# Kernel tuning notes

Hardware: AMD Instinct MI355X
Metric: run time of the kernel (lower is better)

The kernel has to match this reference:

```python
import jax, jax.numpy as jnp
import numpy as np

N, DIN, DH, DOUT, E, K = 8192, 1024, 4096, 1024, 8, 2
AUX_EPS = 1e-10


def setup_inputs() -> dict:
    key = jax.random.key(0)
    kx, kgw, kgb, kw1, kb1, kw2, kb2 = jax.random.split(key, 7)
    def init(k, shape, fan_in):
        return (jax.random.normal(k, shape, jnp.float32) / np.sqrt(fan_in)).astype(jnp.float32)
    return {
        "x": jax.random.normal(kx, (N, DIN), jnp.float32),
        "gate_w": init(kgw, (DIN, E), DIN),
        "gate_b": jnp.zeros((E,), jnp.float32),
        "w1": init(kw1, (E, DIN, DH), DIN),
        "b1": jnp.zeros((E, DH), jnp.float32),
        "w2": init(kw2, (E, DH, DOUT), DH),
        "b2": jnp.zeros((E, DOUT), jnp.float32),
    }


def reference(x, gate_w, gate_b, w1, b1, w2, b2):
    # Gating
    logits = x @ gate_w + gate_b                      # [N, E]
    probs = jax.nn.softmax(logits, axis=-1)           # [N, E]
    topk_vals, topk_idx = jax.lax.top_k(probs, K)     # [N, K]
    topk_norm = topk_vals / (topk_vals.sum(-1, keepdims=True) + AUX_EPS)

    # Scatter normalized top-k weights into a dense [N, E] combine matrix.
    n = x.shape[0]
    weights = jnp.zeros((n, E), x.dtype).at[jnp.arange(n)[:, None], topk_idx].add(topk_norm)

    # Dense all-expert FFN (same math: non-selected experts get weight 0).
    h = jax.nn.relu(jnp.einsum('nd,edh->neh', x, w1) + b1)   # [N, E, DH]
    y = jnp.einsum('neh,eho->neo', h, w2) + b2               # [N, E, DOUT]
    output = jnp.einsum('neo,ne->no', y, weights)            # [N, DOUT]

    # Aux load-balancing loss: KL(mean_probs || uniform)
    mean_probs = probs.mean(axis=0)
    aux_loss = jnp.sum(mean_probs * jnp.log(mean_probs * E + AUX_EPS))

    return output, aux_loss, probs
```

## Files before the change

kernel.cpp:

```cpp
#include <hip/hip_runtime.h>

#define NTOK 8192
#define DIN 1024
#define DH   4096
#define DOUT 1024
#define NE   8
#define MAXTILES 136
#define SLOTCAP  (MAXTILES*128)

typedef __bf16 bf16x8 __attribute__((ext_vector_type(8)));
typedef float  f32x4  __attribute__((ext_vector_type(4)));

constexpr size_t OFF_W1T  = 0;
constexpr size_t OFF_W2T  = 67108864;
constexpr size_t OFF_XB   = 134217728;
constexpr size_t OFF_H    = 150994944;
constexpr size_t OFF_SROW = 293601280;
constexpr size_t OFF_SW   = 293670912;
constexpr size_t OFF_TIDX = 293740544;
constexpr size_t OFF_TW   = 293806080;
constexpr size_t OFF_CTRL = 293871616;
constexpr size_t OFF_PART = 293871744;

__device__ __forceinline__ ushort f2bf(float f){
  unsigned u = __float_as_uint(f);
  u += 0x7fff + ((u >> 16) & 1);
  return (ushort)(u >> 16);
}

#define GLDS(g,l) __builtin_amdgcn_global_load_lds( \
    (const __attribute__((address_space(1))) void*)(g), \
    (__attribute__((address_space(3))) void*)(l), 16, 0, 0)

__global__ void k_cvt_x(const float4* __restrict__ x, ushort4* __restrict__ xb){
  int i = blockIdx.x * 256 + threadIdx.x;
  float4 v = x[i];
  ushort4 o;
  o.x = f2bf(v.x); o.y = f2bf(v.y); o.z = f2bf(v.z); o.w = f2bf(v.w);
  xb[i] = o;
}

__global__ void k_transpose(const float* __restrict__ W, ushort* __restrict__ WT, int R, int C){
  __shared__ ushort tl[64][65];
  int e  = blockIdx.z;
  int r0 = blockIdx.x * 64, c0 = blockIdx.y * 64;
  const float* Wp  = W  + (size_t)e * R * C;
  ushort*      WTp = WT + (size_t)e * R * C;
  int tr = threadIdx.x >> 6, tc = threadIdx.x & 63;
#pragma unroll
  for (int i = 0; i < 16; i++){
    int r = tr + i * 4;
    tl[r][tc] = f2bf(Wp[(size_t)(r0 + r) * C + c0 + tc]);
  }
  __syncthreads();
#pragma unroll
  for (int i = 0; i < 16; i++){
    int r = tr + i * 4;
    WTp[(size_t)(c0 + r) * R + r0 + tc] = tl[tc][r];
  }
}

__global__ void k_gate(const float* __restrict__ x, const float* __restrict__ gw,
                       const float* __restrict__ gb, float* __restrict__ probs_out,
                       int* __restrict__ topk_idx, float* __restrict__ topk_w,
                       int* __restrict__ count, float* __restrict__ partial){
  __shared__ float psum[8];
  __shared__ int   pcnt[8];
  int wv = threadIdx.x >> 6, lane = threadIdx.x & 63;
  int row = blockIdx.x * 4 + wv;
  if (threadIdx.x < 8){ psum[threadIdx.x] = 0.f; pcnt[threadIdx.x] = 0; }
  __syncthreads();

  const float4* x4 = (const float4*)(x + (size_t)row * DIN);
  float acc[8];
#pragma unroll
  for (int e = 0; e < 8; e++) acc[e] = 0.f;
#pragma unroll
  for (int j = 0; j < 4; j++){
    float4 v = x4[j * 64 + lane];
    int kbase = (j * 64 + lane) * 4;
#pragma unroll
    for (int c = 0; c < 4; c++){
      float xv = (&v.x)[c];
      const float4* g4 = (const float4*)(gw + (size_t)(kbase + c) * 8);
      float4 g0 = g4[0], g1 = g4[1];
      acc[0] += xv * g0.x; acc[1] += xv * g0.y; acc[2] += xv * g0.z; acc[3] += xv * g0.w;
      acc[4] += xv * g1.x; acc[5] += xv * g1.y; acc[6] += xv * g1.z; acc[7] += xv * g1.w;
    }
  }
#pragma unroll
  for (int e = 0; e < 8; e++)
#pragma unroll
    for (int off = 32; off; off >>= 1) acc[e] += __shfl_xor(acc[e], off, 64);

  float lg[8], p[8], mx = -1e30f, s = 0.f;
#pragma unroll
  for (int e = 0; e < 8; e++){ lg[e] = acc[e] + gb[e]; mx = fmaxf(mx, lg[e]); }
#pragma unroll
  for (int e = 0; e < 8; e++){ p[e] = expf(lg[e] - mx); s += p[e]; }
  float inv = 1.f / s;
#pragma unroll
  for (int e = 0; e < 8; e++) p[e] *= inv;

  if (lane < 8) probs_out[(size_t)row * 8 + lane] = p[lane];

  if (lane == 0){
    int i1 = 0; float v1 = p[0];
#pragma unroll
    for (int e = 1; e < 8; e++) if (p[e] > v1){ v1 = p[e]; i1 = e; }
    int i2 = -1; float v2 = -1.f;
#pragma unroll
    for (int e = 0; e < 8; e++){ if (e == i1) continue; if (p[e] > v2){ v2 = p[e]; i2 = e; } }
    float denom = 1.f / (v1 + v2 + 1e-10f);
    topk_idx[row * 2]     = i1;  topk_idx[row * 2 + 1] = i2;
    topk_w  [row * 2]     = v1 * denom;  topk_w[row * 2 + 1] = v2 * denom;
    atomicAdd(&pcnt[i1], 1); atomicAdd(&pcnt[i2], 1);
  }
  if (lane < 8) atomicAdd(&psum[lane], p[lane]);
  __syncthreads();
  if (threadIdx.x < 8){
    partial[(size_t)blockIdx.x * 8 + threadIdx.x] = psum[threadIdx.x];
    if (pcnt[threadIdx.x]) atomicAdd(&count[threadIdx.x], pcnt[threadIdx.x]);
  }
}

__global__ void k_aux(const float* __restrict__ partial, const int* __restrict__ count,
                      float* __restrict__ aux_out, int* __restrict__ tile_off){
  __shared__ float red[256];
  __shared__ float tot[8];
  int t = threadIdx.x, e = t & 7;
  float s = 0.f;
  for (int b = (t >> 3); b < 2048; b += 32) s += partial[(size_t)b * 8 + e];
  red[t] = s; __syncthreads();
  if (t < 8){ float v = 0.f; for (int c = 0; c < 32; c++) v += red[c * 8 + t]; tot[t] = v; }
  __syncthreads();
  if (t == 0){
    float aux = 0.f;
    for (int i = 0; i < 8; i++){
      float m = tot[i] * (1.f / 8192.f);
      aux += m * logf(m * 8.f + 1e-10f);
    }
    aux_out[0] = aux;
    int off = 0;
    for (int i = 0; i < 8; i++){ tile_off[i] = off; off += (count[i] + 127) >> 7; }
    tile_off[8] = off;
  }
}

__global__ void k_scatter(const int* __restrict__ topk_idx, const float* __restrict__ topk_w,
                          const int* __restrict__ tile_off, int* __restrict__ fill,
                          int* __restrict__ slot_row, float* __restrict__ slot_w){
  int i = blockIdx.x * 256 + threadIdx.x;
  int row = i >> 1;
  int e = topk_idx[i];
  float w = topk_w[i];
  int lane = threadIdx.x & 63;
  int pos = 0;
#pragma unroll
  for (int ex = 0; ex < 8; ex++){
    unsigned long long mask = __ballot(e == ex);
    if (e == ex){
      int leader = __ffsll((long long)mask) - 1;
      int base = 0;
      if (lane == leader) base = atomicAdd(&fill[ex], (int)__popcll(mask));
      base = __shfl(base, leader, 64);
      pos = base + (int)__popcll(mask & ((1ull << lane) - 1ull));
    }
  }
  int slot = tile_off[e] * 128 + pos;
  slot_row[slot] = row;
  slot_w[slot]   = w;
}

__global__ __launch_bounds__(256) void k_gemm1(
    const ushort* __restrict__ xb, const ushort* __restrict__ w1t,
    const float* __restrict__ b1, const int* __restrict__ slot_row,
    const int* __restrict__ tile_off, ushort* __restrict__ H){
  __shared__ ushort As[128 * 32];
  __shared__ ushort Bs[128 * 32];
  int tileM = blockIdx.x, tileN = blockIdx.y;
  if (tileM >= tile_off[8]) return;
  int e = 0;
  while (e < 7 && tile_off[e + 1] <= tileM) e++;
  int m0 = tileM * 128, n0 = tileN * 128;
  int t = threadIdx.x;

  const ushort* aBase[2]; const ushort* bBase[2];
#pragma unroll
  for (int i = 0; i < 2; i++){
    int c = i * 256 + t, r = c >> 2, cc = c & 3;
    aBase[i] = xb  + (size_t)slot_row[m0 + r] * DIN + cc * 8;
    bBase[i] = w1t + ((size_t)e * DH + n0 + r) * DIN + cc * 8;
  }
  int wv = t >> 6, lane = t & 63;
  int wm = wv >> 1, wn = wv & 1, quad = lane >> 4, lc = lane & 15;
  f32x4 acc[4][4] = {};

  for (int k0 = 0; k0 < DIN; k0 += 32){
#pragma unroll
    for (int i = 0; i < 2; i++){
      int c = i * 256 + t;
      GLDS(aBase[i] + k0, As + c * 8);
      GLDS(bBase[i] + k0, Bs + c * 8);
    }
    __syncthreads();
    bf16x8 a[4], b[4];
#pragma unroll
    for (int i = 0; i < 4; i++) a[i] = *(const bf16x8*)(As + (wm * 64 + i * 16 + lc) * 32 + quad * 8);
#pragma unroll
    for (int j = 0; j < 4; j++) b[j] = *(const bf16x8*)(Bs + (wn * 64 + j * 16 + lc) * 32 + quad * 8);
#pragma unroll
    for (int i = 0; i < 4; i++)
#pragma unroll
      for (int j = 0; j < 4; j++)
        acc[i][j] = __builtin_amdgcn_mfma_f32_16x16x32_bf16(a[i], b[j], acc[i][j], 0, 0, 0);
    __syncthreads();
  }

  const float* b1e = b1 + (size_t)e * DH;
#pragma unroll
  for (int i = 0; i < 4; i++){
#pragma unroll
    for (int r = 0; r < 4; r++){
      int slot = m0 + wm * 64 + i * 16 + quad * 4 + r;
      ushort* hrow = H + (size_t)slot * DH;
#pragma unroll
      for (int j = 0; j < 4; j++){
        int col = n0 + wn * 64 + j * 16 + lc;
        float v = acc[i][j][r] + b1e[col];
        hrow[col] = f2bf(fmaxf(v, 0.f));
      }
    }
  }
}

__global__ __launch_bounds__(256) void k_gemm2(
    const ushort* __restrict__ H, const ushort* __restrict__ w2t,
    const float* __restrict__ b2, const int* __restrict__ slot_row,
    const float* __restrict__ slot_w, const int* __restrict__ tile_off,
    float* __restrict__ out){
  __shared__ ushort As[128 * 32];
  __shared__ ushort Bs[128 * 32];
  int tileM = blockIdx.x, tileN = blockIdx.y;
  if (tileM >= tile_off[8]) return;
  int e = 0;
  while (e < 7 && tile_off[e + 1] <= tileM) e++;
  int m0 = tileM * 128, n0 = tileN * 128;
  int t = threadIdx.x;

  const ushort* aBase[2]; const ushort* bBase[2];
#pragma unroll
  for (int i = 0; i < 2; i++){
    int c = i * 256 + t, r = c >> 2, cc = c & 3;
    aBase[i] = H   + (size_t)(m0 + r) * DH + cc * 8;
    bBase[i] = w2t + ((size_t)e * DOUT + n0 + r) * DH + cc * 8;
  }
  int wv = t >> 6, lane = t & 63;
  int wm = wv >> 1, wn = wv & 1, quad = lane >> 4, lc = lane & 15;
  f32x4 acc[4][4] = {};

  for (int k0 = 0; k0 < DH; k0 += 32){
#pragma unroll
    for (int i = 0; i < 2; i++){
      int c = i * 256 + t;
      GLDS(aBase[i] + k0, As + c * 8);
      GLDS(bBase[i] + k0, Bs + c * 8);
    }
    __syncthreads();
    bf16x8 a[4], b[4];
#pragma unroll
    for (int i = 0; i < 4; i++) a[i] = *(const bf16x8*)(As + (wm * 64 + i * 16 + lc) * 32 + quad * 8);
#pragma unroll
    for (int j = 0; j < 4; j++) b[j] = *(const bf16x8*)(Bs + (wn * 64 + j * 16 + lc) * 32 + quad * 8);
#pragma unroll
    for (int i = 0; i < 4; i++)
#pragma unroll
      for (int j = 0; j < 4; j++)
        acc[i][j] = __builtin_amdgcn_mfma_f32_16x16x32_bf16(a[i], b[j], acc[i][j], 0, 0, 0);
    __syncthreads();
  }

  const float* b2e = b2 + (size_t)e * DOUT;
#pragma unroll
  for (int i = 0; i < 4; i++){
#pragma unroll
    for (int r = 0; r < 4; r++){
      int slot = m0 + wm * 64 + i * 16 + quad * 4 + r;
      float w = slot_w[slot];
      if (w == 0.f) continue;
      float* orow = out + (size_t)slot_row[slot] * DOUT;
#pragma unroll
      for (int j = 0; j < 4; j++){
        int col = n0 + wn * 64 + j * 16 + lc;
        atomicAdd(orow + col, w * (acc[i][j][r] + b2e[col]));
      }
    }
  }
}

extern "C" void kernel_launch(void* const* d_in, const int* in_sizes, int n_in,
                              void* d_out, int out_size, void* d_ws, size_t ws_size,
                              hipStream_t stream){
  const float* x      = (const float*)d_in[0];
  const float* gate_w = (const float*)d_in[1];
  const float* gate_b = (const float*)d_in[2];
  const float* w1     = (const float*)d_in[3];
  const float* b1     = (const float*)d_in[4];
  const float* w2     = (const float*)d_in[5];
  const float* b2     = (const float*)d_in[6];
  float* out = (float*)d_out;

  char* ws = (char*)d_ws;
  ushort* W1T   = (ushort*)(ws + OFF_W1T);
  ushort* W2T   = (ushort*)(ws + OFF_W2T);
  ushort* XB    = (ushort*)(ws + OFF_XB);
  ushort* H     = (ushort*)(ws + OFF_H);
  int*    SROW  = (int*)   (ws + OFF_SROW);
  float*  SW    = (float*) (ws + OFF_SW);
  int*    TIDX  = (int*)   (ws + OFF_TIDX);
  float*  TW    = (float*) (ws + OFF_TW);
  int*    COUNT = (int*)   (ws + OFF_CTRL);
  int*    FILL  = (int*)   (ws + OFF_CTRL + 32);
  int*    TOFF  = (int*)   (ws + OFF_CTRL + 64);
  float*  PART  = (float*) (ws + OFF_PART);

  float* aux_out   = out + (size_t)NTOK * DOUT;
  float* probs_out = aux_out + 1;

  hipMemsetAsync(d_out, 0, (size_t)out_size * 4, stream);
  hipMemsetAsync(ws + OFF_CTRL, 0, 128, stream);
  hipMemsetAsync(ws + OFF_SROW, 0, (size_t)SLOTCAP * 8, stream);

  k_cvt_x<<<dim3((NTOK * DIN / 4) / 256), 256, 0, stream>>>((const float4*)x, (ushort4*)XB);
  k_transpose<<<dim3(DIN / 64, DH / 64, NE), 256, 0, stream>>>(w1, W1T, DIN, DH);
  k_transpose<<<dim3(DH / 64, DOUT / 64, NE), 256, 0, stream>>>(w2, W2T, DH, DOUT);
  k_gate<<<dim3(NTOK / 4), 256, 0, stream>>>(x, gate_w, gate_b, probs_out, TIDX, TW, COUNT, PART);
  k_aux<<<dim3(1), 256, 0, stream>>>(PART, COUNT, aux_out, TOFF);
  k_scatter<<<dim3(NTOK * 2 / 256), 256, 0, stream>>>(TIDX, TW, TOFF, FILL, SROW, SW);
  k_gemm1<<<dim3(MAXTILES, DH / 128), 256, 0, stream>>>(XB, W1T, b1, SROW, TOFF, H);
  k_gemm2<<<dim3(MAXTILES, DOUT / 128), 256, 0, stream>>>(H, W2T, b2, SROW, SW, TOFF, out);
}
```

Measured before the change: 990.4 us.

## Replace grouped GEMMs with 256-row tiled, double-buffered, swizzled 8-wave kernel

Both expert GEMMs now use one templated kernel with 256-row M tiles, 512 threads, a double-buffered LDS pipeline with XOR-swizzled layout, staged global-to-LDS prefetch interleaved with MFMA clusters, s_setprio, and an XCD-aware block remap. Routing tiles are padded to 256 rows, and the W1/W2 transposed buffers now share one workspace region, with the W2 transpose run after GEMM1. The aim is more data reuse per tile, fewer LDS bank conflicts and hidden load latency. The cost is extra padding waste per expert and higher register pressure.

Result: slower. 1.353 ms (+36.6%).

```diff
diff --git a/kernel.cpp b/kernel.cpp
--- a/kernel.cpp
+++ b/kernel.cpp
@@ -1,26 +1,25 @@
 #include <hip/hip_runtime.h>
 
 #define NTOK 8192
-#define DIN 1024
+#define DIN  1024
 #define DH   4096
 #define DOUT 1024
 #define NE   8
-#define MAXTILES 136
-#define SLOTCAP  (MAXTILES*128)
+#define MAXT 72
+#define SLOTCAP (MAXT*256)
 
 typedef __bf16 bf16x8 __attribute__((ext_vector_type(8)));
 typedef float  f32x4  __attribute__((ext_vector_type(4)));
 
-constexpr size_t OFF_W1T  = 0;
-constexpr size_t OFF_W2T  = 67108864;
-constexpr size_t OFF_XB   = 134217728;
-constexpr size_t OFF_H    = 150994944;
-constexpr size_t OFF_SROW = 293601280;
-constexpr size_t OFF_SW   = 293670912;
-constexpr size_t OFF_TIDX = 293740544;
-constexpr size_t OFF_TW   = 293806080;
-constexpr size_t OFF_CTRL = 293871616;
-constexpr size_t OFF_PART = 293871744;
+constexpr size_t OFF_WT   = 0;
+constexpr size_t OFF_XB   = 67108864;
+constexpr size_t OFF_H    = 83886080;
+constexpr size_t OFF_SROW = 234881024;
+constexpr size_t OFF_SW   = 234954752;
+constexpr size_t OFF_TIDX = 235028480;
+constexpr size_t OFF_TW   = 235094016;
+constexpr size_t OFF_CTRL = 235159552;
+constexpr size_t OFF_PART = 235159680;
 
 __device__ __forceinline__ ushort f2bf(float f){
   unsigned u = __float_as_uint(f);
@@ -31,6 +30,10 @@
 #define GLDS(g,l) __builtin_amdgcn_global_load_lds( \
     (const __attribute__((address_space(1))) void*)(g), \
     (__attribute__((address_space(3))) void*)(l), 16, 0, 0)
+
+#define SBAR __builtin_amdgcn_sched_barrier(0)
+#define WBAR __builtin_amdgcn_s_barrier()
+#define VMCNT(n) asm volatile("s_waitcnt vmcnt(" #n ")" ::: "memory")
 
 __global__ void k_cvt_x(const float4* __restrict__ x, ushort4* __restrict__ xb){
   int i = blockIdx.x * 256 + threadIdx.x;
@@ -142,7 +145,7 @@
     }
     aux_out[0] = aux;
     int off = 0;
-    for (int i = 0; i < 8; i++){ tile_off[i] = off; off += (count[i] + 127) >> 7; }
+    for (int i = 0; i < 8; i++){ tile_off[i] = off; off += (count[i] + 255) >> 8; }
     tile_off[8] = off;
   }
 }
@@ -167,134 +170,172 @@
       pos = base + (int)__popcll(mask & ((1ull << lane) - 1ull));
     }
   }
-  int slot = tile_off[e] * 128 + pos;
+  int slot = tile_off[e] * 256 + pos;
   slot_row[slot] = row;
   slot_w[slot]   = w;
 }
 
-__global__ __launch_bounds__(256) void k_gemm1(
-    const ushort* __restrict__ xb, const ushort* __restrict__ w1t,
-    const float* __restrict__ b1, const int* __restrict__ slot_row,
-    const int* __restrict__ tile_off, ushort* __restrict__ H){
-  __shared__ ushort As[128 * 32];
-  __shared__ ushort Bs[128 * 32];
-  int tileM = blockIdx.x, tileN = blockIdx.y;
+#define READ_A(dst, mh, kk) do {                                          \
+  _Pragma("unroll")                                                       \
+  for (int i_ = 0; i_ < 4; i_++)                                          \
+    dst[i_] = *(const bf16x8*)(Ab + aRowBase + ((mh)*4 + i_)*1024 + (foff ^ ((kk)*32))); \
+} while(0)
+
+#define READ_Bf(dst, kk) do {                                             \
+  _Pragma("unroll")                                                       \
+  for (int nj_ = 0; nj_ < NREP; nj_++)                                    \
+    dst[nj_] = *(const bf16x8*)(Bb + bRowBase + nj_*1024 + (foff ^ ((kk)*32))); \
+} while(0)
+
+#define MFMA_CL(aset, bset, mh) do {                                      \
+  __builtin_amdgcn_s_setprio(1);                                          \
+  _Pragma("unroll")                                                       \
+  for (int i_ = 0; i_ < 4; i_++)                                          \
+    _Pragma("unroll")                                                     \
+    for (int nj_ = 0; nj_ < NREP; nj_++)                                  \
+      acc[(mh)*4 + i_][nj_] = __builtin_amdgcn_mfma_f32_16x16x32_bf16(    \
+          aset[i_], bset[nj_], acc[(mh)*4 + i_][nj_], 0, 0, 0);           \
+  __builtin_amdgcn_s_setprio(0);                                          \
+} while(0)
+
+template<int KDIM, int NTOTAL, int NREP, int MODE>
+__global__ __launch_bounds__(512, 2) void k_gemm8(
+    const ushort* __restrict__ Ag, const ushort* __restrict__ Wt,
+    const float* __restrict__ bias, const int* __restrict__ slot_row,
+    const float* __restrict__ slot_w, const int* __restrict__ tile_off,
+    ushort* __restrict__ Hout, float* __restrict__ out)
+{
+  constexpr int BN = NREP * 64;
+  constexpr int NTN = NTOTAL / BN;
+  constexpr int NT = KDIM / 64;
+  constexpr int BQ = NREP;
+
+  __shared__ __align__(16) ushort As[2][256 * 64];
+  __shared__ __align__(16) ushort Bs[2][BN * 64];
+
+  int nwg = gridDim.x, orig = blockIdx.x;
+  int q = nwg >> 3, r8 = nwg & 7;
+  int xcd = orig & 7, loc = orig >> 3;
+  int wg = (xcd < r8 ? xcd * (q + 1) : r8 * (q + 1) + (xcd - r8) * q) + loc;
+  int tileM = wg / NTN, tileN = wg - tileM * NTN;
   if (tileM >= tile_off[8]) return;
   int e = 0;
   while (e < 7 && tile_off[e + 1] <= tileM) e++;
-  int m0 = tileM * 128, n0 = tileN * 128;
+  int m0 = tileM * 256, n0 = tileN * BN;
   int t = threadIdx.x;
-
-  const ushort* aBase[2]; const ushort* bBase[2];
-#pragma unroll
-  for (int i = 0; i < 2; i++){
-    int c = i * 256 + t, r = c >> 2, cc = c & 3;
-    aBase[i] = xb  + (size_t)slot_row[m0 + r] * DIN + cc * 8;
-    bBase[i] = w1t + ((size_t)e * DH + n0 + r) * DIN + cc * 8;
-  }
-  int wv = t >> 6, lane = t & 63;
-  int wm = wv >> 1, wn = wv & 1, quad = lane >> 4, lc = lane & 15;
-  f32x4 acc[4][4] = {};
-
-  for (int k0 = 0; k0 < DIN; k0 += 32){
-#pragma unroll
-    for (int i = 0; i < 2; i++){
-      int c = i * 256 + t;
-      GLDS(aBase[i] + k0, As + c * 8);
-      GLDS(bBase[i] + k0, Bs + c * 8);
-    }
-    __syncthreads();
-    bf16x8 a[4], b[4];
-#pragma unroll
-    for (int i = 0; i < 4; i++) a[i] = *(const bf16x8*)(As + (wm * 64 + i * 16 + lc) * 32 + quad * 8);
-#pragma unroll
-    for (int j = 0; j < 4; j++) b[j] = *(const bf16x8*)(Bs + (wn * 64 + j * 16 + lc) * 32 + quad * 8);
-#pragma unroll
-    for (int i = 0; i < 4; i++)
-#pragma unroll
-      for (int j = 0; j < 4; j++)
-        acc[i][j] = __builtin_amdgcn_mfma_f32_16x16x32_bf16(a[i], b[j], acc[i][j], 0, 0, 0);
-    __syncthreads();
-  }
-
-  const float* b1e = b1 + (size_t)e * DH;
+  int lane = t & 63, wv = t >> 6, quad = lane >> 4, lc = lane & 15;
+  int wm = wv >> 2, wn = wv & 3;
+
+  const ushort* aSrc[4];
 #pragma unroll
   for (int i = 0; i < 4; i++){
-#pragma unroll
-    for (int r = 0; r < 4; r++){
-      int slot = m0 + wm * 64 + i * 16 + quad * 4 + r;
-      ushort* hrow = H + (size_t)slot * DH;
-#pragma unroll
-      for (int j = 0; j < 4; j++){
-        int col = n0 + wn * 64 + j * 16 + lc;
-        float v = acc[i][j][r] + b1e[col];
-        hrow[col] = f2bf(fmaxf(v, 0.f));
+    int c = i * 512 + t, rr = c >> 3;
+    int o = ((c & 7) * 16) ^ ((rr & 7) << 4);
+    size_t rowbase = (MODE == 0) ? (size_t)slot_row[m0 + rr] * KDIM
+                                 : (size_t)(m0 + rr) * KDIM;
+    aSrc[i] = Ag + rowbase + (o >> 1);
+  }
+  const ushort* bSrc[BQ];
+#pragma unroll
+  for (int i = 0; i < BQ; i++){
+    int c = i * 512 + t, rr = c >> 3;
+    int o = ((c & 7) * 16) ^ ((rr & 7) << 4);
+    bSrc[i] = Wt + ((size_t)e * NTOTAL + n0 + rr) * (size_t)KDIM + (o >> 1);
+  }
+
+  int foff = ((quad * 16) ^ ((lc & 7) << 4)) >> 1;
+  int aRowBase = (wm * 128 + lc) * 64;
+  int bRowBase = (wn * (NREP * 16) + lc) * 64;
+
+  f32x4 acc[8][NREP] = {};
+  bf16x8 a0[4], a1[4], b0[NREP], b1[NREP];
+
+#pragma unroll
+  for (int i = 0; i < 4; i++) GLDS(aSrc[i], &As[0][(i * 512 + t) * 8]);
+#pragma unroll
+  for (int i = 0; i < BQ; i++) GLDS(bSrc[i], &Bs[0][(i * 512 + t) * 8]);
+
+  for (int kt = 0; kt < NT; ++kt){
+    const int cur = kt & 1, nxt = cur ^ 1;
+    const ushort* Ab = &As[cur][0];
+    const ushort* Bb = &Bs[cur][0];
+    ushort* Ad = &As[nxt][0];
+    ushort* Bd = &Bs[nxt][0];
+    const int ko = (kt + 1) * 64;
+    const bool pf = (kt + 1 < NT);
+
+    if (pf){
+      GLDS(aSrc[0] + ko, Ad + (0 * 512 + t) * 8);
+      GLDS(bSrc[0] + ko, Bd + (0 * 512 + t) * 8);
+      SBAR;
+      VMCNT(2);
+    } else {
+      SBAR;
+      VMCNT(0);
+    }
+    SBAR; WBAR; SBAR;
+
+    READ_Bf(b0, 0);
+    READ_A(a0, 0, 0);
+    MFMA_CL(a0, b0, 0);
+    if (pf){
+      GLDS(aSrc[1] + ko, Ad + (1 * 512 + t) * 8);
+      if constexpr (BQ > 1) GLDS(bSrc[1] + ko, Bd + (1 * 512 + t) * 8);
+    }
+    READ_A(a1, 1, 0);
+    SBAR; WBAR; SBAR;
+
+    MFMA_CL(a1, b0, 1);
+    if (pf){
+      GLDS(aSrc[2] + ko, Ad + (2 * 512 + t) * 8);
+      if constexpr (BQ > 2) GLDS(bSrc[2] + ko, Bd + (2 * 512 + t) * 8);
+    }
+    READ_Bf(b1, 1);
+    READ_A(a0, 0, 1);
+    SBAR; WBAR; SBAR;
+
+    MFMA_CL(a0, b1, 0);
+    if (pf){
+      GLDS(aSrc[3] + ko, Ad + (3 * 512 + t) * 8);
+      if constexpr (BQ > 3) GLDS(bSrc[3] + ko, Bd + (3 * 512 + t) * 8);
+    }
+    READ_A(a1, 1, 1);
+    SBAR; WBAR; SBAR;
+
+    MFMA_CL(a1, b1, 1);
+    SBAR; WBAR; SBAR;
+  }
+
+  const float* be = bias + (size_t)e * NTOTAL;
+  if constexpr (MODE == 0){
+#pragma unroll
+    for (int mi = 0; mi < 8; mi++)
+#pragma unroll
+      for (int rr = 0; rr < 4; rr++){
+        int slot = m0 + wm * 128 + mi * 16 + quad * 4 + rr;
+        ushort* hrow = Hout + (size_t)slot * NTOTAL;
+#pragma unroll
+        for (int nj = 0; nj < NREP; nj++){
+          int col = n0 + wn * (NREP * 16) + nj * 16 + lc;
+          float v = acc[mi][nj][rr] + be[col];
+          hrow[col] = f2bf(fmaxf(v, 0.f));
+        }
       }
-    }
-  }
-}
-
-__global__ __launch_bounds__(256) void k_gemm2(
-    const ushort* __restrict__ H, const ushort* __restrict__ w2t,
-    const float* __restrict__ b2, const int* __restrict__ slot_row,
-    const float* __restrict__ slot_w, const int* __restrict__ tile_off,
-    float* __restrict__ out){
-  __shared__ ushort As[128 * 32];
-  __shared__ ushort Bs[128 * 32];
-  int tileM = blockIdx.x, tileN = blockIdx.y;
-  if (tileM >= tile_off[8]) return;
-  int e = 0;
-  while (e < 7 && tile_off[e + 1] <= tileM) e++;
-  int m0 = tileM * 128, n0 = tileN * 128;
-  int t = threadIdx.x;
-
-  const ushort* aBase[2]; const ushort* bBase[2];
-#pragma unroll
-  for (int i = 0; i < 2; i++){
-    int c = i * 256 + t, r = c >> 2, cc = c & 3;
-    aBase[i] = H   + (size_t)(m0 + r) * DH + cc * 8;
-    bBase[i] = w2t + ((size_t)e * DOUT + n0 + r) * DH + cc * 8;
-  }
-  int wv = t >> 6, lane = t & 63;
-  int wm = wv >> 1, wn = wv & 1, quad = lane >> 4, lc = lane & 15;
-  f32x4 acc[4][4] = {};
-
-  for (int k0 = 0; k0 < DH; k0 += 32){
-#pragma unroll
-    for (int i = 0; i < 2; i++){
-      int c = i * 256 + t;
-      GLDS(aBase[i] + k0, As + c * 8);
-      GLDS(bBase[i] + k0, Bs + c * 8);
-    }
-    __syncthreads();
-    bf16x8 a[4], b[4];
-#pragma unroll
-    for (int i = 0; i < 4; i++) a[i] = *(const bf16x8*)(As + (wm * 64 + i * 16 + lc) * 32 + quad * 8);
-#pragma unroll
-    for (int j = 0; j < 4; j++) b[j] = *(const bf16x8*)(Bs + (wn * 64 + j * 16 + lc) * 32 + quad * 8);
-#pragma unroll
-    for (int i = 0; i < 4; i++)
-#pragma unroll
-      for (int j = 0; j < 4; j++)
-        acc[i][j] = __builtin_amdgcn_mfma_f32_16x16x32_bf16(a[i], b[j], acc[i][j], 0, 0, 0);
-    __syncthreads();
-  }
-
-  const float* b2e = b2 + (size_t)e * DOUT;
-#pragma unroll
-  for (int i = 0; i < 4; i++){
-#pragma unroll
-    for (int r = 0; r < 4; r++){
-      int slot = m0 + wm * 64 + i * 16 + quad * 4 + r;
-      float w = slot_w[slot];
-      if (w == 0.f) continue;
-      float* orow = out + (size_t)slot_row[slot] * DOUT;
-#pragma unroll
-      for (int j = 0; j < 4; j++){
-        int col = n0 + wn * 64 + j * 16 + lc;
-        atomicAdd(orow + col, w * (acc[i][j][r] + b2e[col]));
+  } else {
+#pragma unroll
+    for (int mi = 0; mi < 8; mi++)
+#pragma unroll
+      for (int rr = 0; rr < 4; rr++){
+        int slot = m0 + wm * 128 + mi * 16 + quad * 4 + rr;
+        float w = slot_w[slot];
+        if (w == 0.f) continue;
+        float* orow = out + (size_t)slot_row[slot] * NTOTAL;
+#pragma unroll
+        for (int nj = 0; nj < NREP; nj++){
+          int col = n0 + wn * (NREP * 16) + nj * 16 + lc;
+          atomicAdd(orow + col, w * (acc[mi][nj][rr] + be[col]));
+        }
       }
-    }
   }
 }
 
@@ -311,8 +352,7 @@
   float* out = (float*)d_out;
 
   char* ws = (char*)d_ws;
-  ushort* W1T   = (ushort*)(ws + OFF_W1T);
-  ushort* W2T   = (ushort*)(ws + OFF_W2T);
+  ushort* WT    = (ushort*)(ws + OFF_WT);
   ushort* XB    = (ushort*)(ws + OFF_XB);
   ushort* H     = (ushort*)(ws + OFF_H);
   int*    SROW  = (int*)   (ws + OFF_SROW);
@@ -332,11 +372,16 @@
   hipMemsetAsync(ws + OFF_SROW, 0, (size_t)SLOTCAP * 8, stream);
 
   k_cvt_x<<<dim3((NTOK * DIN / 4) / 256), 256, 0, stream>>>((const float4*)x, (ushort4*)XB);
-  k_transpose<<<dim3(DIN / 64, DH / 64, NE), 256, 0, stream>>>(w1, W1T, DIN, DH);
-  k_transpose<<<dim3(DH / 64, DOUT / 64, NE), 256, 0, stream>>>(w2, W2T, DH, DOUT);
+  k_transpose<<<dim3(DIN / 64, DH / 64, NE), 256, 0, stream>>>(w1, WT, DIN, DH);
   k_gate<<<dim3(NTOK / 4), 256, 0, stream>>>(x, gate_w, gate_b, probs_out, TIDX, TW, COUNT, PART);
   k_aux<<<dim3(1), 256, 0, stream>>>(PART, COUNT, aux_out, TOFF);
   k_scatter<<<dim3(NTOK * 2 / 256), 256, 0, stream>>>(TIDX, TW, TOFF, FILL, SROW, SW);
-  k_gemm1<<<dim3(MAXTILES, DH / 128), 256, 0, stream>>>(XB, W1T, b1, SROW, TOFF, H);
-  k_gemm2<<<dim3(MAXTILES, DOUT / 128), 256, 0, stream>>>(H, W2T, b2, SROW, SW, TOFF, out);
-}
+
+  k_gemm8<DIN, DH, 4, 0><<<dim3(MAXT * (DH / 256)), 512, 0, stream>>>(
+      XB, WT, b1, SROW, SW, TOFF, H, nullptr);
+
+  k_transpose<<<dim3(DH / 64, DOUT / 64, NE), 256, 0, stream>>>(w2, WT, DH, DOUT);
+
+  k_gemm8<DH, DOUT, 2, 1><<<dim3(MAXT * (DOUT / 128)), 512, 0, stream>>>(
+      H, WT, b2, SROW, SW, TOFF, nullptr, out);
+}
```
